# Performance work log

Hardware: AMD Instinct MI355X
Metric: run time of the kernel (lower is better)

Reference implementation:

```python
import jax, jax.numpy as jnp
import numpy as np

HID, H, VD = 512, 8, 64
SCALE = 1.0 / np.sqrt(VD).astype(np.float32)


def setup_inputs() -> dict:
    key = jax.random.key(0)
    ks = jax.random.split(key, 9)
    B, S = 2, 2048
    std = 1.0 / np.sqrt(HID).astype(np.float32)
    return {
        "sequences": jax.random.normal(ks[0], (B, S, HID), jnp.float32),
        "Wq": jax.random.normal(ks[1], (H, HID, VD), jnp.float32) * std,
        "bq": jax.random.normal(ks[2], (H, VD), jnp.float32) * std,
        "Wk": jax.random.normal(ks[3], (H, HID, VD), jnp.float32) * std,
        "bk": jax.random.normal(ks[4], (H, VD), jnp.float32) * std,
        "Wv": jax.random.normal(ks[5], (H, HID, VD), jnp.float32) * std,
        "bv": jax.random.normal(ks[6], (H, VD), jnp.float32) * std,
        "Wo": jax.random.normal(ks[7], (HID, HID), jnp.float32) * std,
        "bo": jax.random.normal(ks[8], (HID,), jnp.float32) * std,
    }


def reference(sequences, Wq, bq, Wk, bk, Wv, bv, Wo, bo):
    # Batched equivalent of the per-sequence / per-head Python loops:
    # q,k,v: [B, H, S, VD]
    q = jnp.einsum("bsd,hde->bhse", sequences, Wq) + bq[None, :, None, :]
    k = jnp.einsum("bsd,hde->bhse", sequences, Wk) + bk[None, :, None, :]
    v = jnp.einsum("bsd,hde->bhse", sequences, Wv) + bv[None, :, None, :]
    scores = jax.nn.softmax(jnp.einsum("bhse,bhte->bhst", q, k) * SCALE, axis=-1)
    z = jnp.einsum("bhst,bhte->bhse", scores, v)  # [B,H,S,VD]
    # concat heads along feature dim -> [B, S, HID]
    B, _, S, _ = z.shape
    z = jnp.transpose(z, (0, 2, 1, 3)).reshape(B, S, HID)
    return z @ Wo + bo
```

## Files before the change

### kernel.cpp

```cpp
#include <hip/hip_runtime.h>
#include <hip/hip_fp16.h>

#define HID 512
#define NH 8
#define VD 64
#define SEQ 2048
#define NB 2
#define MTOT (NB*SEQ)
#define LOG2E 1.4426950408889634f
#define QSCALE (0.125f * LOG2E)

typedef _Float16 f16x8 __attribute__((ext_vector_type(8)));
typedef _Float16 f16x4 __attribute__((ext_vector_type(4)));
typedef float f32x4 __attribute__((ext_vector_type(4)));

#define OFF_SEQH  (0u)
#define SZ_SEQH   ((unsigned)(MTOT*HID*2))
#define OFF_WT    (OFF_SEQH + SZ_SEQH)
#define SZ_WT     ((unsigned)(3*NH*VD*HID*2))
#define OFF_WOT   (OFF_WT + SZ_WT)
#define SZ_WOT    ((unsigned)(HID*HID*2))
#define OFF_BIAS  (OFF_WOT + SZ_WOT)
#define SZ_BIAS   ((unsigned)(3*NH*VD*4))
#define OFF_Q     (OFF_BIAS + SZ_BIAS)
#define SZ_QKV    ((unsigned)(NB*NH*SEQ*VD*2))
#define OFF_K     (OFF_Q + SZ_QKV)
#define OFF_VT    (OFF_K + SZ_QKV)
#define OFF_Z     (OFF_VT + SZ_QKV)

__device__ __forceinline__ int swz(int row, int g) {
    return row*128 + ((g ^ (row & 7)) << 4);
}
__device__ __forceinline__ int swz256(int row, int g) {
    return row*256 + ((g ^ (row & 7)) << 4);
}

__global__ __launch_bounds__(256) void k_convert(
    const float* __restrict__ seq,
    const float* __restrict__ Wq, const float* __restrict__ bq,
    const float* __restrict__ Wk, const float* __restrict__ bk,
    const float* __restrict__ Wv, const float* __restrict__ bv,
    const float* __restrict__ Wo, char* __restrict__ ws)
{
    int tid = blockIdx.x*256 + threadIdx.x;
    int nt  = gridDim.x*256;

    _Float16* seqh = (_Float16*)(ws + OFF_SEQH);
    for (int i = tid; i < MTOT*HID/4; i += nt) {
        float4 v = ((const float4*)seq)[i];
        f16x4 o = { (_Float16)v.x, (_Float16)v.y, (_Float16)v.z, (_Float16)v.w };
        ((f16x4*)seqh)[i] = o;
    }

    _Float16* wt = (_Float16*)(ws + OFF_WT);
    for (int i = tid; i < 3*NH*VD*HID; i += nt) {
        int k = i & (HID-1); int t = i >> 9;
        int vd = t & (VD-1); t >>= 6;
        int h = t & (NH-1);  int z = t >> 3;
        const float* W = (z==0) ? Wq : (z==1 ? Wk : Wv);
        wt[i] = (_Float16)W[(h*HID + k)*VD + vd];
    }

    _Float16* wot = (_Float16*)(ws + OFF_WOT);
    for (int i = tid; i < HID*HID; i += nt) {
        int k = i & (HID-1); int n = i >> 9;
        wot[i] = (_Float16)Wo[k*HID + n];
    }

    float* bias = (float*)(ws + OFF_BIAS);
    for (int i = tid; i < 3*NH*VD; i += nt) {
        int z = i / (NH*VD); int r = i % (NH*VD);
        const float* b = (z==0) ? bq : (z==1 ? bk : bv);
        bias[i] = b[r];
    }
}

__global__ __launch_bounds__(256) void k_proj(char* __restrict__ ws)
{
    __shared__ uint4 smem4[1536];
    char* smem = (char*)smem4;
    const _Float16* seqh = (const _Float16*)(ws + OFF_SEQH);
    const _Float16* wt   = (const _Float16*)(ws + OFF_WT);
    const float*    bias = (const float*)(ws + OFF_BIAS);

    int m0 = blockIdx.x * 128;
    int h  = blockIdx.y;
    int z  = blockIdx.z;
    int tid = threadIdx.x, lane = tid & 63, w = tid >> 6;

    f32x4 acc[2][4] = {};

    for (int kt = 0; kt < HID/64; ++kt) {
        #pragma unroll
        for (int p = 0; p < 4; ++p) {
            int flat = p*256 + tid; int row = flat >> 3, g = flat & 7;
            uint4 v = *(const uint4*)(seqh + (m0+row)*HID + kt*64 + g*8);
            *(uint4*)(smem + swz(row, g)) = v;
        }
        #pragma unroll
        for (int p = 0; p < 2; ++p) {
            int flat = p*256 + tid; int n = flat >> 3, g = flat & 7;
            uint4 v = *(const uint4*)(wt + ((z*NH+h)*VD + n)*HID + kt*64 + g*8);
            *(uint4*)(smem + 16384 + swz(n, g)) = v;
        }
        __syncthreads();
        #pragma unroll
        for (int kf = 0; kf < 2; ++kf) {
            f16x8 a[2], b[4];
            #pragma unroll
            for (int mf = 0; mf < 2; ++mf) {
                int row = w*32 + mf*16 + (lane & 15);
                a[mf] = *(const f16x8*)(smem + swz(row, kf*4 + (lane>>4)));
            }
            #pragma unroll
            for (int nf = 0; nf < 4; ++nf) {
                int n = nf*16 + (lane & 15);
                b[nf] = *(const f16x8*)(smem + 16384 + swz(n, kf*4 + (lane>>4)));
            }
            #pragma unroll
            for (int mf = 0; mf < 2; ++mf)
                #pragma unroll
                for (int nf = 0; nf < 4; ++nf)
                    acc[mf][nf] = __builtin_amdgcn_mfma_f32_16x16x32_f16(
                        a[mf], b[nf], acc[mf][nf], 0, 0, 0);
        }
        __syncthreads();
    }

    int bb = m0 >> 11;
    int s0 = m0 & (SEQ-1);

    if (z < 2) {
        float sc = (z == 0) ? QSCALE : 1.0f;
        _Float16* out = (_Float16*)(ws + (z==0 ? OFF_Q : OFF_K));
        #pragma unroll
        for (int mf = 0; mf < 2; ++mf)
            #pragma unroll
            for (int nf = 0; nf < 4; ++nf)
                #pragma unroll
                for (int r = 0; r < 4; ++r) {
                    int mrow = w*32 + mf*16 + ((lane>>4)<<2) + r;
                    int col  = nf*16 + (lane & 15);
                    float v = (acc[mf][nf][r] + bias[(z*NH+h)*VD + col]) * sc;
                    out[((bb*NH+h)*SEQ + s0 + mrow)*VD + col] = (_Float16)v;
                }
    } else {
        _Float16* sT = (_Float16*)smem;
        #pragma unroll
        for (int mf = 0; mf < 2; ++mf)
            #pragma unroll
            for (int nf = 0; nf < 4; ++nf)
                #pragma unroll
                for (int r = 0; r < 4; ++r) {
                    int srow = w*32 + mf*16 + ((lane>>4)<<2) + r;
                    int vd   = nf*16 + (lane & 15);
                    float v = acc[mf][nf][r] + bias[(z*NH+h)*VD + vd];
                    sT[vd*128 + srow] = (_Float16)v;
                }
        __syncthreads();
        _Float16* vt = (_Float16*)(ws + OFF_VT);
        #pragma unroll
        for (int p = 0; p < 4; ++p) {
            int flat = p*256 + tid; int vd = flat >> 4, g = flat & 15;
            uint4 v = *(const uint4*)((char*)sT + vd*256 + g*16);
            *(uint4*)(vt + ((bb*NH+h)*VD + vd)*SEQ + s0 + g*8) = v;
        }
    }
}

__global__ __launch_bounds__(256, 3) void k_attn(char* __restrict__ ws)
{
    __shared__ uint4 smem4[3072];
    char* smem = (char*)smem4;
    const int OK = 0, OV = 16384, OP = 32768;

    int m0 = blockIdx.x * 64;
    int bh = blockIdx.y;
    int tid = threadIdx.x, lane = tid & 63, w = tid >> 6;

    const _Float16* Qb  = (const _Float16*)(ws + OFF_Q)  + (unsigned)bh*SEQ*VD;
    const _Float16* Kb  = (const _Float16*)(ws + OFF_K)  + (unsigned)bh*SEQ*VD;
    const _Float16* Vtb = (const _Float16*)(ws + OFF_VT) + (unsigned)bh*VD*SEQ;
    _Float16* Zp = (_Float16*)(ws + OFF_Z);

    f16x8 aq[2];
    #pragma unroll
    for (int kf = 0; kf < 2; ++kf)
        aq[kf] = *(const f16x8*)(Qb + (m0 + w*16 + (lane & 15))*VD
                                 + kf*32 + (lane>>4)*8);

    float mrun[4], lrun[4];
    f32x4 zacc[4] = {};
    #pragma unroll
    for (int r = 0; r < 4; ++r) { mrun[r] = -INFINITY; lrun[r] = 0.f; }

    for (int t0 = 0; t0 < SEQ; t0 += 128) {
        #pragma unroll
        for (int p = 0; p < 4; ++p) {
            int flat = p*256 + tid; int r = flat >> 3, g = flat & 7;
            uint4 v = *(const uint4*)(Kb + (t0+r)*VD + g*8);
            *(uint4*)(smem + OK + swz(r, g)) = v;
        }
        #pragma unroll
        for (int p = 0; p < 4; ++p) {
            int flat = p*256 + tid; int r = flat >> 4, g = flat & 15;
            uint4 v = *(const uint4*)(Vtb + r*SEQ + t0 + g*8);
            *(uint4*)(smem + OV + swz256(r, g)) = v;
        }
        __syncthreads();

        f32x4 sacc[8] = {};
        #pragma unroll
        for (int kf = 0; kf < 2; ++kf) {
            f16x8 bk_[8];
            #pragma unroll
            for (int nf = 0; nf < 8; ++nf) {
                int trow = nf*16 + (lane & 15);
                bk_[nf] = *(const f16x8*)(smem + OK + swz(trow, kf*4 + (lane>>4)));
            }
            #pragma unroll
            for (int nf = 0; nf < 8; ++nf)
                sacc[nf] = __builtin_amdgcn_mfma_f32_16x16x32_f16(
                    aq[kf], bk_[nf], sacc[nf], 0, 0, 0);
        }

        #pragma unroll
        for (int r = 0; r < 4; ++r) {
            float v = fmaxf(fmaxf(fmaxf(sacc[0][r], sacc[1][r]),
                                  fmaxf(sacc[2][r], sacc[3][r])),
                            fmaxf(fmaxf(sacc[4][r], sacc[5][r]),
                                  fmaxf(sacc[6][r], sacc[7][r])));
            #pragma unroll
            for (int d = 1; d < 16; d <<= 1) v = fmaxf(v, __shfl_xor(v, d, 64));
            if (v > mrun[r] + 8.0f) {
                float al = __builtin_amdgcn_exp2f(mrun[r] - v);
                mrun[r] = v;
                lrun[r] *= al;
                #pragma unroll
                for (int nf = 0; nf < 4; ++nf) zacc[nf][r] *= al;
            }
            float s = 0.f;
            #pragma unroll
            for (int nf = 0; nf < 8; ++nf) {
                float p = __builtin_amdgcn_exp2f(sacc[nf][r] - mrun[r]);
                sacc[nf][r] = p;
                s += p;
            }
            #pragma unroll
            for (int d = 1; d < 16; d <<= 1) s += __shfl_xor(s, d, 64);
            lrun[r] += s;
        }

        #pragma unroll
        for (int nf = 0; nf < 8; ++nf)
            #pragma unroll
            for (int r = 0; r < 4; ++r) {
                int row = w*16 + ((lane>>4)<<2) + r;
                int g   = nf*2 + ((lane>>3) & 1);
                *(_Float16*)(smem + OP + row*256 + ((g ^ (row & 7))<<4)
                             + (lane & 7)*2) = (_Float16)sacc[nf][r];
            }

        #pragma unroll
        for (int kf = 0; kf < 4; ++kf) {
            int prow = w*16 + (lane & 15);
            f16x8 ap = *(const f16x8*)(smem + OP + swz256(prow, kf*4 + (lane>>4)));
            f16x8 bv_[4];
            #pragma unroll
            for (int nf = 0; nf < 4; ++nf) {
                int vd = nf*16 + (lane & 15);
                bv_[nf] = *(const f16x8*)(smem + OV + swz256(vd, kf*4 + (lane>>4)));
            }
            #pragma unroll
            for (int nf = 0; nf < 4; ++nf)
                zacc[nf] = __builtin_amdgcn_mfma_f32_16x16x32_f16(
                    ap, bv_[nf], zacc[nf], 0, 0, 0);
        }
        __syncthreads();
    }

    int bb = bh >> 3, h = bh & 7;
    float linv[4];
    #pragma unroll
    for (int r = 0; r < 4; ++r) linv[r] = 1.0f / lrun[r];
    #pragma unroll
    for (int nf = 0; nf < 4; ++nf)
        #pragma unroll
        for (int r = 0; r < 4; ++r) {
            int s  = m0 + w*16 + ((lane>>4)<<2) + r;
            int vd = nf*16 + (lane & 15);
            float v = zacc[nf][r] * linv[r];
            Zp[((unsigned)(bb*SEQ + s))*HID + h*VD + vd] = (_Float16)v;
        }
}

__global__ __launch_bounds__(256) void k_outproj(const char* __restrict__ ws,
                                                 const float* __restrict__ bo,
                                                 float* __restrict__ out)
{
    __shared__ uint4 smem4[1536];
    char* smem = (char*)smem4;
    const _Float16* Zp  = (const _Float16*)(ws + OFF_Z);
    const _Float16* wot = (const _Float16*)(ws + OFF_WOT);

    int m0 = blockIdx.x * 128;
    int n0 = blockIdx.y * 64;
    int tid = threadIdx.x, lane = tid & 63, w = tid >> 6;

    f32x4 acc[2][4] = {};

    for (int kt = 0; kt < HID/64; ++kt) {
        #pragma unroll
        for (int p = 0; p < 4; ++p) {
            int flat = p*256 + tid; int row = flat >> 3, g = flat & 7;
            uint4 v = *(const uint4*)(Zp + (m0+row)*HID + kt*64 + g*8);
            *(uint4*)(smem + swz(row, g)) = v;
        }
        #pragma unroll
        for (int p = 0; p < 2; ++p) {
            int flat = p*256 + tid; int n = flat >> 3, g = flat & 7;
            uint4 v = *(const uint4*)(wot + (n0+n)*HID + kt*64 + g*8);
            *(uint4*)(smem + 16384 + swz(n, g)) = v;
        }
        __syncthreads();
        #pragma unroll
        for (int kf = 0; kf < 2; ++kf) {
            f16x8 a[2], b[4];
            #pragma unroll
            for (int mf = 0; mf < 2; ++mf) {
                int row = w*32 + mf*16 + (lane & 15);
                a[mf] = *(const f16x8*)(smem + swz(row, kf*4 + (lane>>4)));
            }
            #pragma unroll
            for (int nf = 0; nf < 4; ++nf) {
                int n = nf*16 + (lane & 15);
                b[nf] = *(const f16x8*)(smem + 16384 + swz(n, kf*4 + (lane>>4)));
            }
            #pragma unroll
            for (int mf = 0; mf < 2; ++mf)
                #pragma unroll
                for (int nf = 0; nf < 4; ++nf)
                    acc[mf][nf] = __builtin_amdgcn_mfma_f32_16x16x32_f16(
                        a[mf], b[nf], acc[mf][nf], 0, 0, 0);
        }
        __syncthreads();
    }

    #pragma unroll
    for (int mf = 0; mf < 2; ++mf)
        #pragma unroll
        for (int nf = 0; nf < 4; ++nf)
            #pragma unroll
            for (int r = 0; r < 4; ++r) {
                int mrow = m0 + w*32 + mf*16 + ((lane>>4)<<2) + r;
                int col  = n0 + nf*16 + (lane & 15);
                out[(unsigned)mrow*HID + col] = acc[mf][nf][r] + bo[col];
            }
}

extern "C" void kernel_launch(void* const* d_in, const int* in_sizes, int n_in,
                              void* d_out, int out_size, void* d_ws, size_t ws_size,
                              hipStream_t stream)
{
    const float* seq = (const float*)d_in[0];
    const float* Wq  = (const float*)d_in[1];
    const float* bq  = (const float*)d_in[2];
    const float* Wk  = (const float*)d_in[3];
    const float* bk  = (const float*)d_in[4];
    const float* Wv  = (const float*)d_in[5];
    const float* bv  = (const float*)d_in[6];
    const float* Wo  = (const float*)d_in[7];
    const float* bo  = (const float*)d_in[8];
    char* ws = (char*)d_ws;
    float* out = (float*)d_out;

    k_convert<<<dim3(512), dim3(256), 0, stream>>>(seq, Wq, bq, Wk, bk, Wv, bv, Wo, ws);
    k_proj<<<dim3(32, 8, 3), dim3(256), 0, stream>>>(ws);
    k_attn<<<dim3(32, 16), dim3(256), 0, stream>>>(ws);
    k_outproj<<<dim3(32, 8), dim3(256), 0, stream>>>(ws, bo, out);
}
```

Before: 153.1 us.

## Double-buffer K/V tiles in attention, tile weight transposes through LDS

The attention kernel now uses 64-key tiles with register-prefetched double buffering in LDS, so the next tile's global loads overlap the current tile's MFMA and softmax work. It needs only one barrier per iteration, uses less LDS and allows four blocks per CU. The convert kernel now transposes the QKV and output weights through an LDS tile with coalesced float4 reads and 16-byte writes, replacing strided per-element gathers. Bias staging is dropped and k_proj reads the biases directly. Smaller key tiles mean more loop iterations and more softmax rescale overhead per key.

Result: slower. 193.1 us (+26.1%).

```diff
diff --git a/kernel.cpp b/kernel.cpp
--- a/kernel.cpp
+++ b/kernel.cpp
@@ -31,62 +31,91 @@
 __device__ __forceinline__ int swz(int row, int g) {
     return row*128 + ((g ^ (row & 7)) << 4);
 }
-__device__ __forceinline__ int swz256(int row, int g) {
-    return row*256 + ((g ^ (row & 7)) << 4);
-}
 
 __global__ __launch_bounds__(256) void k_convert(
     const float* __restrict__ seq,
-    const float* __restrict__ Wq, const float* __restrict__ bq,
-    const float* __restrict__ Wk, const float* __restrict__ bk,
-    const float* __restrict__ Wv, const float* __restrict__ bv,
-    const float* __restrict__ Wo, char* __restrict__ ws)
+    const float* __restrict__ Wq, const float* __restrict__ Wk,
+    const float* __restrict__ Wv, const float* __restrict__ Wo,
+    char* __restrict__ ws)
 {
-    int tid = blockIdx.x*256 + threadIdx.x;
-    int nt  = gridDim.x*256;
-
-    _Float16* seqh = (_Float16*)(ws + OFF_SEQH);
-    for (int i = tid; i < MTOT*HID/4; i += nt) {
-        float4 v = ((const float4*)seq)[i];
-        f16x4 o = { (_Float16)v.x, (_Float16)v.y, (_Float16)v.z, (_Float16)v.w };
-        ((f16x4*)seqh)[i] = o;
-    }
-
-    _Float16* wt = (_Float16*)(ws + OFF_WT);
-    for (int i = tid; i < 3*NH*VD*HID; i += nt) {
-        int k = i & (HID-1); int t = i >> 9;
-        int vd = t & (VD-1); t >>= 6;
-        int h = t & (NH-1);  int z = t >> 3;
+    __shared__ _Float16 lt[64][72];
+    int bx = blockIdx.x, tid = threadIdx.x;
+
+    if (bx < 192) {
+        int z = bx / 64, h = (bx & 63) >> 3, kt = bx & 7;
         const float* W = (z==0) ? Wq : (z==1 ? Wk : Wv);
-        wt[i] = (_Float16)W[(h*HID + k)*VD + vd];
-    }
-
-    _Float16* wot = (_Float16*)(ws + OFF_WOT);
-    for (int i = tid; i < HID*HID; i += nt) {
-        int k = i & (HID-1); int n = i >> 9;
-        wot[i] = (_Float16)Wo[k*HID + n];
-    }
-
-    float* bias = (float*)(ws + OFF_BIAS);
-    for (int i = tid; i < 3*NH*VD; i += nt) {
-        int z = i / (NH*VD); int r = i % (NH*VD);
-        const float* b = (z==0) ? bq : (z==1 ? bk : bv);
-        bias[i] = b[r];
-    }
-}
-
-__global__ __launch_bounds__(256) void k_proj(char* __restrict__ ws)
+        int k0 = kt*64;
+        #pragma unroll
+        for (int p = 0; p < 4; ++p) {
+            int flat = p*256 + tid;
+            int kr = flat >> 4, c4 = flat & 15;
+            float4 v = *(const float4*)(W + (h*HID + k0 + kr)*VD + c4*4);
+            lt[c4*4+0][kr] = (_Float16)v.x;
+            lt[c4*4+1][kr] = (_Float16)v.y;
+            lt[c4*4+2][kr] = (_Float16)v.z;
+            lt[c4*4+3][kr] = (_Float16)v.w;
+        }
+        __syncthreads();
+        _Float16* wt = (_Float16*)(ws + OFF_WT);
+        #pragma unroll
+        for (int p = 0; p < 2; ++p) {
+            int flat = p*256 + tid;
+            int vd = flat >> 3, gg = flat & 7;
+            f16x8 o;
+            #pragma unroll
+            for (int j = 0; j < 8; ++j) o[j] = lt[vd][gg*8+j];
+            *(f16x8*)(wt + ((z*NH + h)*VD + vd)*HID + k0 + gg*8) = o;
+        }
+    } else if (bx < 256) {
+        int idx = bx - 192, ntile = idx >> 3, kt = idx & 7;
+        int k0 = kt*64, n0 = ntile*64;
+        #pragma unroll
+        for (int p = 0; p < 4; ++p) {
+            int flat = p*256 + tid;
+            int kr = flat >> 4, c4 = flat & 15;
+            float4 v = *(const float4*)(Wo + (k0 + kr)*HID + n0 + c4*4);
+            lt[c4*4+0][kr] = (_Float16)v.x;
+            lt[c4*4+1][kr] = (_Float16)v.y;
+            lt[c4*4+2][kr] = (_Float16)v.z;
+            lt[c4*4+3][kr] = (_Float16)v.w;
+        }
+        __syncthreads();
+        _Float16* wot = (_Float16*)(ws + OFF_WOT);
+        #pragma unroll
+        for (int p = 0; p < 2; ++p) {
+            int flat = p*256 + tid;
+            int nl = flat >> 3, gg = flat & 7;
+            f16x8 o;
+            #pragma unroll
+            for (int j = 0; j < 8; ++j) o[j] = lt[nl][gg*8+j];
+            *(f16x8*)(wot + (n0 + nl)*HID + k0 + gg*8) = o;
+        }
+    } else {
+        int t = (bx - 256)*256 + tid;
+        const float4* s4p = (const float4*)seq;
+        f16x4* d = (f16x4*)(ws + OFF_SEQH);
+        for (int i = t; i < MTOT*HID/4; i += 256*256) {
+            float4 v = s4p[i];
+            f16x4 o = {(_Float16)v.x,(_Float16)v.y,(_Float16)v.z,(_Float16)v.w};
+            d[i] = o;
+        }
+    }
+}
+
+__global__ __launch_bounds__(256) void k_proj(char* __restrict__ ws,
+    const float* __restrict__ bq, const float* __restrict__ bk,
+    const float* __restrict__ bv)
 {
     __shared__ uint4 smem4[1536];
     char* smem = (char*)smem4;
     const _Float16* seqh = (const _Float16*)(ws + OFF_SEQH);
     const _Float16* wt   = (const _Float16*)(ws + OFF_WT);
-    const float*    bias = (const float*)(ws + OFF_BIAS);
 
     int m0 = blockIdx.x * 128;
     int h  = blockIdx.y;
     int z  = blockIdx.z;
     int tid = threadIdx.x, lane = tid & 63, w = tid >> 6;
+    const float* bias = (z==0) ? bq : (z==1 ? bk : bv);
 
     f32x4 acc[2][4] = {};
 
@@ -141,7 +170,7 @@
                 for (int r = 0; r < 4; ++r) {
                     int mrow = w*32 + mf*16 + ((lane>>4)<<2) + r;
                     int col  = nf*16 + (lane & 15);
-                    float v = (acc[mf][nf][r] + bias[(z*NH+h)*VD + col]) * sc;
+                    float v = (acc[mf][nf][r] + bias[h*VD + col]) * sc;
                     out[((bb*NH+h)*SEQ + s0 + mrow)*VD + col] = (_Float16)v;
                 }
     } else {
@@ -154,7 +183,7 @@
                 for (int r = 0; r < 4; ++r) {
                     int srow = w*32 + mf*16 + ((lane>>4)<<2) + r;
                     int vd   = nf*16 + (lane & 15);
-                    float v = acc[mf][nf][r] + bias[(z*NH+h)*VD + vd];
+                    float v = acc[mf][nf][r] + bias[h*VD + vd];
                     sT[vd*128 + srow] = (_Float16)v;
                 }
         __syncthreads();
@@ -168,20 +197,23 @@
     }
 }
 
-__global__ __launch_bounds__(256, 3) void k_attn(char* __restrict__ ws)
+__global__ __launch_bounds__(256, 4) void k_attn(char* __restrict__ ws)
 {
-    __shared__ uint4 smem4[3072];
+    __shared__ uint4 smem4[2560];
     char* smem = (char*)smem4;
-    const int OK = 0, OV = 16384, OP = 32768;
+    const int OP = 32768;
 
     int m0 = blockIdx.x * 64;
     int bh = blockIdx.y;
     int tid = threadIdx.x, lane = tid & 63, w = tid >> 6;
 
-    const _Float16* Qb  = (const _Float16*)(ws + OFF_Q)  + (unsigned)bh*SEQ*VD;
-    const _Float16* Kb  = (const _Float16*)(ws + OFF_K)  + (unsigned)bh*SEQ*VD;
-    const _Float16* Vtb = (const _Float16*)(ws + OFF_VT) + (unsigned)bh*VD*SEQ;
+    const _Float16* Qb  = (const _Float16*)(ws + OFF_Q)  + (size_t)bh*SEQ*VD;
+    const _Float16* Kb  = (const _Float16*)(ws + OFF_K)  + (size_t)bh*SEQ*VD;
+    const _Float16* Vtb = (const _Float16*)(ws + OFF_VT) + (size_t)bh*VD*SEQ;
     _Float16* Zp = (_Float16*)(ws + OFF_Z);
+
+    int r0 = tid >> 3,        g0 = tid & 7;
+    int r1 = (256 + tid) >> 3, g1 = tid & 7;
 
     f16x8 aq[2];
     #pragma unroll
@@ -194,42 +226,51 @@
     #pragma unroll
     for (int r = 0; r < 4; ++r) { mrun[r] = -INFINITY; lrun[r] = 0.f; }
 
-    for (int t0 = 0; t0 < SEQ; t0 += 128) {
-        #pragma unroll
-        for (int p = 0; p < 4; ++p) {
-            int flat = p*256 + tid; int r = flat >> 3, g = flat & 7;
-            uint4 v = *(const uint4*)(Kb + (t0+r)*VD + g*8);
-            *(uint4*)(smem + OK + swz(r, g)) = v;
-        }
-        #pragma unroll
-        for (int p = 0; p < 4; ++p) {
-            int flat = p*256 + tid; int r = flat >> 4, g = flat & 15;
-            uint4 v = *(const uint4*)(Vtb + r*SEQ + t0 + g*8);
-            *(uint4*)(smem + OV + swz256(r, g)) = v;
-        }
-        __syncthreads();
-
-        f32x4 sacc[8] = {};
+    {
+        uint4 ka0 = *(const uint4*)(Kb + (size_t)r0*VD + g0*8);
+        uint4 ka1 = *(const uint4*)(Kb + (size_t)r1*VD + g1*8);
+        uint4 va0 = *(const uint4*)(Vtb + (size_t)r0*SEQ + g0*8);
+        uint4 va1 = *(const uint4*)(Vtb + (size_t)r1*SEQ + g1*8);
+        *(uint4*)(smem + swz(r0, g0)) = ka0;
+        *(uint4*)(smem + swz(r1, g1)) = ka1;
+        *(uint4*)(smem + 16384 + swz(r0, g0)) = va0;
+        *(uint4*)(smem + 16384 + swz(r1, g1)) = va1;
+    }
+
+    int cur = 0;
+    for (int t0 = 0; t0 < SEQ; t0 += 64) {
+        __syncthreads();
+
+        bool more = (t0 + 64 < SEQ);
+        uint4 ka0, ka1, va0, va1;
+        if (more) {
+            ka0 = *(const uint4*)(Kb + (size_t)(t0+64+r0)*VD + g0*8);
+            ka1 = *(const uint4*)(Kb + (size_t)(t0+64+r1)*VD + g1*8);
+            va0 = *(const uint4*)(Vtb + (size_t)r0*SEQ + t0+64 + g0*8);
+            va1 = *(const uint4*)(Vtb + (size_t)r1*SEQ + t0+64 + g1*8);
+        }
+
+        const int OK = cur*8192, OV = 16384 + cur*8192;
+
+        f32x4 sacc[4] = {};
         #pragma unroll
         for (int kf = 0; kf < 2; ++kf) {
-            f16x8 bk_[8];
-            #pragma unroll
-            for (int nf = 0; nf < 8; ++nf) {
+            f16x8 bk_[4];
+            #pragma unroll
+            for (int nf = 0; nf < 4; ++nf) {
                 int trow = nf*16 + (lane & 15);
                 bk_[nf] = *(const f16x8*)(smem + OK + swz(trow, kf*4 + (lane>>4)));
             }
             #pragma unroll
-            for (int nf = 0; nf < 8; ++nf)
+            for (int nf = 0; nf < 4; ++nf)
                 sacc[nf] = __builtin_amdgcn_mfma_f32_16x16x32_f16(
                     aq[kf], bk_[nf], sacc[nf], 0, 0, 0);
         }
 
         #pragma unroll
         for (int r = 0; r < 4; ++r) {
-            float v = fmaxf(fmaxf(fmaxf(sacc[0][r], sacc[1][r]),
-                                  fmaxf(sacc[2][r], sacc[3][r])),
-                            fmaxf(fmaxf(sacc[4][r], sacc[5][r]),
-                                  fmaxf(sacc[6][r], sacc[7][r])));
+            float v = fmaxf(fmaxf(sacc[0][r], sacc[1][r]),
+                            fmaxf(sacc[2][r], sacc[3][r]));
             #pragma unroll
             for (int d = 1; d < 16; d <<= 1) v = fmaxf(v, __shfl_xor(v, d, 64));
             if (v > mrun[r] + 8.0f) {
@@ -241,7 +282,7 @@
             }
             float s = 0.f;
             #pragma unroll
-            for (int nf = 0; nf < 8; ++nf) {
+            for (int nf = 0; nf < 4; ++nf) {
                 float p = __builtin_amdgcn_exp2f(sacc[nf][r] - mrun[r]);
                 sacc[nf][r] = p;
                 s += p;
@@ -252,31 +293,39 @@
         }
 
         #pragma unroll
-        for (int nf = 0; nf < 8; ++nf)
+        for (int nf = 0; nf < 4; ++nf)
             #pragma unroll
             for (int r = 0; r < 4; ++r) {
                 int row = w*16 + ((lane>>4)<<2) + r;
                 int g   = nf*2 + ((lane>>3) & 1);
-                *(_Float16*)(smem + OP + row*256 + ((g ^ (row & 7))<<4)
+                *(_Float16*)(smem + OP + row*128 + ((g ^ (row & 7))<<4)
                              + (lane & 7)*2) = (_Float16)sacc[nf][r];
             }
 
         #pragma unroll
-        for (int kf = 0; kf < 4; ++kf) {
+        for (int kf = 0; kf < 2; ++kf) {
             int prow = w*16 + (lane & 15);
-            f16x8 ap = *(const f16x8*)(smem + OP + swz256(prow, kf*4 + (lane>>4)));
+            f16x8 ap = *(const f16x8*)(smem + OP + swz(prow, kf*4 + (lane>>4)));
             f16x8 bv_[4];
             #pragma unroll
             for (int nf = 0; nf < 4; ++nf) {
                 int vd = nf*16 + (lane & 15);
-                bv_[nf] = *(const f16x8*)(smem + OV + swz256(vd, kf*4 + (lane>>4)));
+                bv_[nf] = *(const f16x8*)(smem + OV + swz(vd, kf*4 + (lane>>4)));
             }
             #pragma unroll
             for (int nf = 0; nf < 4; ++nf)
                 zacc[nf] = __builtin_amdgcn_mfma_f32_16x16x32_f16(
                     ap, bv_[nf], zacc[nf], 0, 0, 0);
         }
-        __syncthreads();
+
+        if (more) {
+            int OKn = (cur^1)*8192, OVn = 16384 + (cur^1)*8192;
+            *(uint4*)(smem + OKn + swz(r0, g0)) = ka0;
+            *(uint4*)(smem + OKn + swz(r1, g1)) = ka1;
+            *(uint4*)(smem + OVn + swz(r0, g0)) = va0;
+            *(uint4*)(smem + OVn + swz(r1, g1)) = va1;
+        }
+        cur ^= 1;
     }
 
     int bb = bh >> 3, h = bh & 7;
@@ -290,7 +339,7 @@
             int s  = m0 + w*16 + ((lane>>4)<<2) + r;
             int vd = nf*16 + (lane & 15);
             float v = zacc[nf][r] * linv[r];
-            Zp[((unsigned)(bb*SEQ + s))*HID + h*VD + vd] = (_Float16)v;
+            Zp[((size_t)(bb*SEQ + s))*HID + h*VD + vd] = (_Float16)v;
         }
 }
 
@@ -374,8 +423,8 @@
     char* ws = (char*)d_ws;
     float* out = (float*)d_out;
 
-    k_convert<<<dim3(512), dim3(256), 0, stream>>>(seq, Wq, bq, Wk, bk, Wv, bv, Wo, ws);
-    k_proj<<<dim3(32, 8, 3), dim3(256), 0, stream>>>(ws);
+    k_convert<<<dim3(512), dim3(256), 0, stream>>>(seq, Wq, Wk, Wv, Wo, ws);
+    k_proj<<<dim3(32, 8, 3), dim3(256), 0, stream>>>(ws, bq, bk, bv);
     k_attn<<<dim3(32, 16), dim3(256), 0, stream>>>(ws);
     k_outproj<<<dim3(32, 8), dim3(256), 0, stream>>>(ws, bo, out);
 }
```
